# Performance work log

Hardware: AMD Instinct MI355X
Metric: run time of the kernel (lower is better)

## Reference

```python
import jax, jax.numpy as jnp
import numpy as np

N_NODES = 50000
N_EDGES = 800000
D_FEAT = 64
HIDDEN = 128
OUT = 16


def sage_conv(x, src, dst, W_l, W_r, b):
    # PyG SAGEConv (aggr='mean', root_weight=True):
    #   out = lin_l(mean_{j in N(i)} x_j) + lin_r(x_i)
    n = x.shape[0]
    msg = x[src]                                        # [E, d] gather
    agg = jax.ops.segment_sum(msg, dst, num_segments=n) # [N, d]
    deg = jax.ops.segment_sum(jnp.ones((src.shape[0],), x.dtype), dst, num_segments=n)
    mean = agg / jnp.maximum(deg, 1.0)[:, None]         # 0 for isolated nodes
    return mean @ W_l + b + x @ W_r


def setup_inputs() -> dict:
    key = jax.random.key(0)
    ks = jax.random.split(key, 8)
    s = lambda d: 1.0 / np.sqrt(d)
    return {
        "x": jax.random.normal(ks[0], (N_NODES, D_FEAT), dtype=jnp.float32),
        "edge_index": jax.random.randint(ks[1], (2, N_EDGES), 0, N_NODES, dtype=jnp.int32),
        "W1_l": jax.random.normal(ks[2], (D_FEAT, HIDDEN), dtype=jnp.float32) * s(D_FEAT),
        "W1_r": jax.random.normal(ks[3], (D_FEAT, HIDDEN), dtype=jnp.float32) * s(D_FEAT),
        "b1": jnp.zeros((HIDDEN,), dtype=jnp.float32),
        "W2_l": jax.random.normal(ks[4], (HIDDEN, OUT), dtype=jnp.float32) * s(HIDDEN),
        "W2_r": jax.random.normal(ks[5], (HIDDEN, OUT), dtype=jnp.float32) * s(HIDDEN),
        "b2": jnp.zeros((OUT,), dtype=jnp.float32),
    }


def reference(x, edge_index, W1_l, W1_r, b1, W2_l, W2_r, b2):
    src, dst = edge_index[0], edge_index[1]
    h = jax.nn.relu(sage_conv(x, src, dst, W1_l, W1_r, b1))
    h = sage_conv(h, src, dst, W2_l, W2_r, b2)
    # eval-mode path of the original module
    return jax.nn.softmax(h, axis=1)
```

## Files before the change

### kernel.cpp

```cpp
#include <hip/hip_runtime.h>
#include <math.h>

#define N_NODES 50000
#define N_EDGES 800000
#define D_FEAT  64
#define HIDDEN  128
#define OUT     16
#define CAP     64
#define NXCD    8
#define DPG     (N_NODES / NXCD)
#define CSTR    32
#define ABLK    ((N_EDGES / 4 + 255) / 256 * NXCD)
#define PBLK    800

typedef unsigned short ushort_t;
typedef unsigned int uint_t;
typedef __attribute__((ext_vector_type(8))) __bf16 bf16x8;
typedef __attribute__((ext_vector_type(8))) _Float16 half8;
typedef __attribute__((ext_vector_type(4))) float f32x4;

__device__ __forceinline__ void split8(const float* u, bf16x8& ah, bf16x8& al) {
    #pragma unroll
    for (int i = 0; i < 8; ++i) {
        const __bf16 h = (__bf16)u[i];
        ah[i] = h;
        al[i] = (__bf16)(u[i] - (float)h);
    }
}

__global__ __launch_bounds__(256) void prep0_kernel(
        const int* __restrict__ ei,
        uint_t* __restrict__ ep,
        int* __restrict__ cnt) {
    const int idx = blockIdx.x * 256 + threadIdx.x;
    if (idx < N_NODES * CSTR / 4) {
        const int4 z4 = {0, 0, 0, 0};
        ((int4*)cnt)[idx] = z4;
    }
    if (idx < N_EDGES / 4) {
        const int e4 = idx * 4;
        const int4 s = *(const int4*)(ei + e4);
        const int4 d = *(const int4*)(ei + N_EDGES + e4);
        uint4 p;
        p.x = (uint_t)s.x | ((uint_t)d.x << 16);
        p.y = (uint_t)s.y | ((uint_t)d.y << 16);
        p.z = (uint_t)s.z | ((uint_t)d.z << 16);
        p.w = (uint_t)s.w | ((uint_t)d.w << 16);
        *(uint4*)(ep + e4) = p;
    }
}

__global__ __launch_bounds__(256) void mega_kernel(
        const uint_t* __restrict__ ep,
        int* __restrict__ cnt,
        ushort_t* __restrict__ adj,
        const float* __restrict__ x,
        const float* __restrict__ W1l, const float* __restrict__ W1r,
        const float* __restrict__ W2l, const float* __restrict__ W2r,
        _Float16* __restrict__ xh,
        __bf16* __restrict__ Whi1, __bf16* __restrict__ Wlo1,
        __bf16* __restrict__ Whi2, __bf16* __restrict__ Wlo2) {
    const int blk = blockIdx.x;
    if (blk < ABLK) {
        const int g = blk & (NXCD - 1);
        const int b = blk >> 3;
        const int e4 = (b * 256 + threadIdx.x) * 4;
        if (e4 >= N_EDGES) return;
        const uint4 v = *(const uint4*)(ep + e4);
        const uint_t lo = (uint_t)(g * DPG), hi = lo + DPG;
#define PUT(U) { \
        const uint_t d_ = (U) >> 16; \
        if (d_ >= lo && d_ < hi) { \
            int p = atomicAdd(&cnt[d_ * CSTR], 1); \
            if (p < CAP) adj[d_ * CAP + p] = (ushort_t)((U) & 0xFFFFu); \
        } }
        PUT(v.x) PUT(v.y) PUT(v.z) PUT(v.w)
#undef PUT
        return;
    }
    const int idx = (blk - ABLK) * 256 + threadIdx.x;
    if (idx < N_NODES * D_FEAT / 16) {
        const float4* xp = (const float4*)(x + idx * 16);
        const float4 a = xp[0], b = xp[1], c = xp[2], d = xp[3];
        half8 h0, h1;
        h0[0] = (_Float16)a.x; h0[1] = (_Float16)a.y; h0[2] = (_Float16)a.z; h0[3] = (_Float16)a.w;
        h0[4] = (_Float16)b.x; h0[5] = (_Float16)b.y; h0[6] = (_Float16)b.z; h0[7] = (_Float16)b.w;
        h1[0] = (_Float16)c.x; h1[1] = (_Float16)c.y; h1[2] = (_Float16)c.z; h1[3] = (_Float16)c.w;
        h1[4] = (_Float16)d.x; h1[5] = (_Float16)d.y; h1[6] = (_Float16)d.z; h1[7] = (_Float16)d.w;
        *(half8*)(xh + idx * 16) = h0;
        *(half8*)(xh + idx * 16 + 8) = h1;
    }
    if (idx < 16384) {
        const int k = idx >> 7, c = idx & 127;
        const float v = (k < 64) ? W1l[k * HIDDEN + c] : W1r[(k - 64) * HIDDEN + c];
        const int kt = k >> 5, g = (k >> 3) & 3, j = k & 7;
        const int pos = (((kt * 8 + (c >> 4)) * 64) + (g * 16 + (c & 15))) * 8 + j;
        const __bf16 h = (__bf16)v;
        Whi1[pos] = h;
        Wlo1[pos] = (__bf16)(v - (float)h);
    } else if (idx < 20480) {
        const int i2 = idx - 16384;
        const int k = i2 >> 5, c = i2 & 31;
        const float v = (c < 16) ? W2l[k * OUT + c] : W2r[k * OUT + (c - 16)];
        const int kt = k >> 5, g = (k >> 3) & 3, j = k & 7;
        const int pos = (((kt * 2 + (c >> 4)) * 64) + (g * 16 + (c & 15))) * 8 + j;
        const __bf16 h = (__bf16)v;
        Whi2[pos] = h;
        Wlo2[pos] = (__bf16)(v - (float)h);
    }
}

__global__ __launch_bounds__(256) void gather_mean_kernel(
        const _Float16* __restrict__ xh,
        const ushort_t* __restrict__ adj,
        const int* __restrict__ cnt,
        _Float16* __restrict__ meanh) {
    const int w = (blockIdx.x * 256 + threadIdx.x) >> 6;
    if (w >= N_NODES) return;
    const int lane = threadIdx.x & 63;
    const int eg = lane >> 3, fq = lane & 7;
    int deg = cnt[w * CSTR];
    if (deg > CAP) deg = CAP;
    const int start = w * CAP;
    float acc[8];
    #pragma unroll
    for (int i = 0; i < 8; ++i) acc[i] = 0.f;
    int j = eg;
    for (; j + 8 < deg; j += 16) {
        const int s0 = adj[start + j], s1 = adj[start + j + 8];
        const half8 v0 = *(const half8*)(xh + s0 * D_FEAT + 8 * fq);
        const half8 v1 = *(const half8*)(xh + s1 * D_FEAT + 8 * fq);
        #pragma unroll
        for (int i = 0; i < 8; ++i) acc[i] += (float)v0[i] + (float)v1[i];
    }
    if (j < deg) {
        const int s0 = adj[start + j];
        const half8 v0 = *(const half8*)(xh + s0 * D_FEAT + 8 * fq);
        #pragma unroll
        for (int i = 0; i < 8; ++i) acc[i] += (float)v0[i];
    }
    #pragma unroll
    for (int off = 32; off >= 8; off >>= 1) {
        #pragma unroll
        for (int i = 0; i < 8; ++i) acc[i] += __shfl_down(acc[i], off);
    }
    if (lane < 8) {
        const float invd = 1.f / fmaxf((float)deg, 1.f);
        half8 o;
        #pragma unroll
        for (int i = 0; i < 8; ++i) o[i] = (_Float16)(acc[i] * invd);
        *(half8*)(meanh + w * D_FEAT + 8 * fq) = o;
    }
}

__global__ __launch_bounds__(256) void mfma1_kernel(
        const float* __restrict__ x,
        const _Float16* __restrict__ meanh,
        const __bf16* __restrict__ Whi1, const __bf16* __restrict__ Wlo1,
        const __bf16* __restrict__ Whi2, const __bf16* __restrict__ Wlo2,
        const float* __restrict__ b1,
        float* __restrict__ z, float* __restrict__ rbuf) {
    __shared__ float Hs[4][16][132];
    const int w = threadIdx.x >> 6;
    const int l = threadIdx.x & 63;
    const int g = l >> 4;
    const int col = l & 15;
    const int nodebase = blockIdx.x * 64 + w * 16;
    const int nA = nodebase + col;

    f32x4 acc[8];
    #pragma unroll
    for (int ct = 0; ct < 8; ++ct) acc[ct] = (f32x4){0.f, 0.f, 0.f, 0.f};

    #pragma unroll
    for (int kt = 0; kt < 4; ++kt) {
        float u[8];
        #pragma unroll
        for (int i = 0; i < 8; ++i) u[i] = 0.f;
        if (nA < N_NODES) {
            if (kt < 2) {
                const half8 hv = *(const half8*)(meanh + (size_t)nA * 64 + kt * 32 + g * 8);
                #pragma unroll
                for (int i = 0; i < 8; ++i) u[i] = (float)hv[i];
            } else {
                const float* p = x + (size_t)nA * 64 + (kt & 1) * 32 + g * 8;
                const float4 u0 = *(const float4*)p;
                const float4 u1 = *(const float4*)(p + 4);
                u[0] = u0.x; u[1] = u0.y; u[2] = u0.z; u[3] = u0.w;
                u[4] = u1.x; u[5] = u1.y; u[6] = u1.z; u[7] = u1.w;
            }
        }
        bf16x8 ah, al;
        split8(u, ah, al);
        #pragma unroll
        for (int ct = 0; ct < 8; ++ct) {
            const int fo = ((kt * 8 + ct) * 64 + l) * 8;
            const bf16x8 bh = *(const bf16x8*)(Whi1 + fo);
            const bf16x8 bl = *(const bf16x8*)(Wlo1 + fo);
            acc[ct] = __builtin_amdgcn_mfma_f32_16x16x32_bf16(ah, bh, acc[ct], 0, 0, 0);
            acc[ct] = __builtin_amdgcn_mfma_f32_16x16x32_bf16(al, bh, acc[ct], 0, 0, 0);
            acc[ct] = __builtin_amdgcn_mfma_f32_16x16x32_bf16(ah, bl, acc[ct], 0, 0, 0);
        }
    }

    #pragma unroll
    for (int ct = 0; ct < 8; ++ct) {
        const float bv = b1[ct * 16 + col];
        #pragma unroll
        for (int i = 0; i < 4; ++i)
            Hs[w][g * 4 + i][ct * 16 + col] = fmaxf(acc[ct][i] + bv, 0.f);
    }

    f32x4 acc2[2];
    acc2[0] = (f32x4){0.f, 0.f, 0.f, 0.f};
    acc2[1] = (f32x4){0.f, 0.f, 0.f, 0.f};
    #pragma unroll
    for (int kt2 = 0; kt2 < 4; ++kt2) {
        const float* hp = &Hs[w][col][kt2 * 32 + g * 8];
        const float4 u0 = *(const float4*)hp;
        const float4 u1 = *(const float4*)(hp + 4);
        float u[8];
        u[0] = u0.x; u[1] = u0.y; u[2] = u0.z; u[3] = u0.w;
        u[4] = u1.x; u[5] = u1.y; u[6] = u1.z; u[7] = u1.w;
        bf16x8 ah, al;
        split8(u, ah, al);
        #pragma unroll
        for (int ct2 = 0; ct2 < 2; ++ct2) {
            const int fo = ((kt2 * 2 + ct2) * 64 + l) * 8;
            const bf16x8 bh = *(const bf16x8*)(Whi2 + fo);
            const bf16x8 bl = *(const bf16x8*)(Wlo2 + fo);
            acc2[ct2] = __builtin_amdgcn_mfma_f32_16x16x32_bf16(ah, bh, acc2[ct2], 0, 0, 0);
            acc2[ct2] = __builtin_amdgcn_mfma_f32_16x16x32_bf16(al, bh, acc2[ct2], 0, 0, 0);
            acc2[ct2] = __builtin_amdgcn_mfma_f32_16x16x32_bf16(ah, bl, acc2[ct2], 0, 0, 0);
        }
    }
    #pragma unroll
    for (int ct2 = 0; ct2 < 2; ++ct2) {
        float* dst = ct2 ? rbuf : z;
        #pragma unroll
        for (int i = 0; i < 4; ++i) {
            const int node = nodebase + g * 4 + i;
            if (node < N_NODES) dst[node * OUT + col] = acc2[ct2][i];
        }
    }
}

__global__ __launch_bounds__(256) void fused2_kernel(
        const float* __restrict__ z,
        const float* __restrict__ r_in,
        const ushort_t* __restrict__ adj,
        const int* __restrict__ cnt,
        const float* __restrict__ b2,
        float* __restrict__ out) {
    const int w = (blockIdx.x * 256 + threadIdx.x) >> 6;
    if (w >= N_NODES) return;
    const int lane = threadIdx.x & 63;
    const int eg = lane >> 2, kq = lane & 3;
    int deg = cnt[w * CSTR];
    if (deg > CAP) deg = CAP;
    const int start = w * CAP;
    float4 acc = {0.f, 0.f, 0.f, 0.f};
    for (int j = eg; j < deg; j += 16) {
        const float4 v = *(const float4*)(z + adj[start + j] * OUT + 4 * kq);
        acc.x += v.x; acc.y += v.y; acc.z += v.z; acc.w += v.w;
    }
    #pragma unroll
    for (int off = 32; off >= 4; off >>= 1) {
        acc.x += __shfl_down(acc.x, off); acc.y += __shfl_down(acc.y, off);
        acc.z += __shfl_down(acc.z, off); acc.w += __shfl_down(acc.w, off);
    }
    const float invd = 1.f / fmaxf((float)deg, 1.f);
    const float4 rv = *(const float4*)(r_in + w * OUT + 4 * (lane & 3));
    const float4 bv = *(const float4*)(b2 + 4 * (lane & 3));
    float4 s;
    s.x = acc.x * invd + rv.x + bv.x;
    s.y = acc.y * invd + rv.y + bv.y;
    s.z = acc.z * invd + rv.z + bv.z;
    s.w = acc.w * invd + rv.w + bv.w;
    float m = fmaxf(fmaxf(s.x, s.y), fmaxf(s.z, s.w));
    m = fmaxf(m, __shfl_xor(m, 1));
    m = fmaxf(m, __shfl_xor(m, 2));
    float4 e;
    e.x = __expf(s.x - m); e.y = __expf(s.y - m);
    e.z = __expf(s.z - m); e.w = __expf(s.w - m);
    float t = e.x + e.y + e.z + e.w;
    t += __shfl_xor(t, 1);
    t += __shfl_xor(t, 2);
    if (lane < 4) {
        const float it = 1.f / t;
        float4 o;
        o.x = e.x * it; o.y = e.y * it; o.z = e.z * it; o.w = e.w * it;
        *(float4*)(out + w * OUT + 4 * lane) = o;
    }
}

extern "C" void kernel_launch(void* const* d_in, const int* in_sizes, int n_in,
                              void* d_out, int out_size, void* d_ws, size_t ws_size,
                              hipStream_t stream) {
    const float* x   = (const float*)d_in[0];
    const int*   ei  = (const int*)d_in[1];
    const float* W1l = (const float*)d_in[2];
    const float* W1r = (const float*)d_in[3];
    const float* b1  = (const float*)d_in[4];
    const float* W2l = (const float*)d_in[5];
    const float* W2r = (const float*)d_in[6];
    const float* b2  = (const float*)d_in[7];
    float* out = (float*)d_out;

    char* wsB = (char*)d_ws;
    int*       cnt   = (int*)wsB;
    ushort_t*  adj   = (ushort_t*)(wsB + 6400000);
    uint_t*    ep    = (uint_t*)(wsB + 12800000);
    float*     z     = (float*)(wsB + 12800000);
    _Float16*  xh    = (_Float16*)(wsB + 16000000);
    float*     rbuf  = (float*)(wsB + 16000000);
    _Float16*  meanh = (_Float16*)(wsB + 22400000);
    __bf16*    Whi1  = (__bf16*)(wsB + 28800000);
    __bf16*    Wlo1  = Whi1 + 16384;
    __bf16*    Whi2  = Wlo1 + 16384;
    __bf16*    Wlo2  = Whi2 + 4096;

    prep0_kernel<<<(N_NODES * CSTR / 4 + 255) / 256, 256, 0, stream>>>(ei, ep, cnt);
    mega_kernel<<<ABLK + PBLK, 256, 0, stream>>>(ep, cnt, adj, x,
                                                 W1l, W1r, W2l, W2r,
                                                 xh, Whi1, Wlo1, Whi2, Wlo2);
    gather_mean_kernel<<<N_NODES / 4, 256, 0, stream>>>(xh, adj, cnt, meanh);
    mfma1_kernel<<<(N_NODES + 63) / 64, 256, 0, stream>>>(
        x, meanh, Whi1, Wlo1, Whi2, Wlo2, b1, z, rbuf);
    fused2_kernel<<<N_NODES / 4, 256, 0, stream>>>(z, rbuf, adj, cnt, b2, out);
}
```

Before: 105.9 us.

## Build adjacency with LDS atomics over node groups and per-segment slots

Adjacency construction changes from global atomics on strided per-node counters to blocks that each own a group of 782 destination nodes and one eighth of the edges. Degrees are counted with shared-memory atomics and written as per-segment byte counts, so the counter zeroing in prep0 goes away. Each node gets 8 segments of 16 slots, and the gather kernels walk these segment lists. The risk is that every block now scans a whole edge segment (64 groups re-read the edge array), and edges beyond 16 per segment are dropped, which may be rarer or more common than overflow of the old 64-slot cap.

```diff
diff --git a/kernel.cpp b/kernel.cpp
--- a/kernel.cpp
+++ b/kernel.cpp
@@ -6,14 +6,18 @@
 #define D_FEAT  64
 #define HIDDEN  128
 #define OUT     16
-#define CAP     64
-#define NXCD    8
-#define DPG     (N_NODES / NXCD)
-#define CSTR    32
-#define ABLK    ((N_EDGES / 4 + 255) / 256 * NXCD)
+
+#define GROUPS  64
+#define GNODES  782
+#define SPLITE  8
+#define CAPE    16
+#define ESEG    (N_EDGES / SPLITE)
+#define SBLK    (GROUPS * SPLITE)
 #define PBLK    800
+#define ASTR    (SPLITE * CAPE)
 
 typedef unsigned short ushort_t;
+typedef unsigned char uchar_t;
 typedef unsigned int uint_t;
 typedef __attribute__((ext_vector_type(8))) __bf16 bf16x8;
 typedef __attribute__((ext_vector_type(8))) _Float16 half8;
@@ -30,13 +34,8 @@
 
 __global__ __launch_bounds__(256) void prep0_kernel(
         const int* __restrict__ ei,
-        uint_t* __restrict__ ep,
-        int* __restrict__ cnt) {
+        uint_t* __restrict__ ep) {
     const int idx = blockIdx.x * 256 + threadIdx.x;
-    if (idx < N_NODES * CSTR / 4) {
-        const int4 z4 = {0, 0, 0, 0};
-        ((int4*)cnt)[idx] = z4;
-    }
     if (idx < N_EDGES / 4) {
         const int e4 = idx * 4;
         const int4 s = *(const int4*)(ei + e4);
@@ -52,7 +51,7 @@
 
 __global__ __launch_bounds__(256) void mega_kernel(
         const uint_t* __restrict__ ep,
-        int* __restrict__ cnt,
+        uchar_t* __restrict__ cnt8,
         ushort_t* __restrict__ adj,
         const float* __restrict__ x,
         const float* __restrict__ W1l, const float* __restrict__ W1r,
@@ -61,24 +60,37 @@
         __bf16* __restrict__ Whi1, __bf16* __restrict__ Wlo1,
         __bf16* __restrict__ Whi2, __bf16* __restrict__ Wlo2) {
     const int blk = blockIdx.x;
-    if (blk < ABLK) {
-        const int g = blk & (NXCD - 1);
-        const int b = blk >> 3;
-        const int e4 = (b * 256 + threadIdx.x) * 4;
-        if (e4 >= N_EDGES) return;
-        const uint4 v = *(const uint4*)(ep + e4);
-        const uint_t lo = (uint_t)(g * DPG), hi = lo + DPG;
+    if (blk < SBLK) {
+        __shared__ int scnt[GNODES];
+        const int g = blk >> 3;
+        const int e = blk & 7;
+        const int lo = g * GNODES;
+        const int span = ((N_NODES - lo) < GNODES) ? (N_NODES - lo) : GNODES;
+        for (int i = threadIdx.x; i < GNODES; i += 256) scnt[i] = 0;
+        __syncthreads();
+        const uint4* ep4 = (const uint4*)(ep + e * ESEG);
+        for (int i = threadIdx.x; i < ESEG / 4; i += 256) {
+            const uint4 v = ep4[i];
 #define PUT(U) { \
-        const uint_t d_ = (U) >> 16; \
-        if (d_ >= lo && d_ < hi) { \
-            int p = atomicAdd(&cnt[d_ * CSTR], 1); \
-            if (p < CAP) adj[d_ * CAP + p] = (ushort_t)((U) & 0xFFFFu); \
-        } }
-        PUT(v.x) PUT(v.y) PUT(v.z) PUT(v.w)
+            const int d_ = (int)((U) >> 16) - lo; \
+            if ((uint_t)d_ < (uint_t)span) { \
+                const int s_ = atomicAdd(&scnt[d_], 1); \
+                if (s_ < CAPE) \
+                    adj[(size_t)(lo + d_) * ASTR + e * CAPE + s_] = \
+                        (ushort_t)((U) & 0xFFFFu); \
+            } }
+            PUT(v.x) PUT(v.y) PUT(v.z) PUT(v.w)
 #undef PUT
+        }
+        __syncthreads();
+        for (int i = threadIdx.x; i < span; i += 256) {
+            int c = scnt[i];
+            if (c > CAPE) c = CAPE;
+            cnt8[(size_t)(lo + i) * SPLITE + e] = (uchar_t)c;
+        }
         return;
     }
-    const int idx = (blk - ABLK) * 256 + threadIdx.x;
+    const int idx = (blk - SBLK) * 256 + threadIdx.x;
     if (idx < N_NODES * D_FEAT / 16) {
         const float4* xp = (const float4*)(x + idx * 16);
         const float4 a = xp[0], b = xp[1], c = xp[2], d = xp[3];
@@ -93,8 +105,8 @@
     if (idx < 16384) {
         const int k = idx >> 7, c = idx & 127;
         const float v = (k < 64) ? W1l[k * HIDDEN + c] : W1r[(k - 64) * HIDDEN + c];
-        const int kt = k >> 5, g = (k >> 3) & 3, j = k & 7;
-        const int pos = (((kt * 8 + (c >> 4)) * 64) + (g * 16 + (c & 15))) * 8 + j;
+        const int kt = k >> 5, gg = (k >> 3) & 3, j = k & 7;
+        const int pos = (((kt * 8 + (c >> 4)) * 64) + (gg * 16 + (c & 15))) * 8 + j;
         const __bf16 h = (__bf16)v;
         Whi1[pos] = h;
         Wlo1[pos] = (__bf16)(v - (float)h);
@@ -102,8 +114,8 @@
         const int i2 = idx - 16384;
         const int k = i2 >> 5, c = i2 & 31;
         const float v = (c < 16) ? W2l[k * OUT + c] : W2r[k * OUT + (c - 16)];
-        const int kt = k >> 5, g = (k >> 3) & 3, j = k & 7;
-        const int pos = (((kt * 2 + (c >> 4)) * 64) + (g * 16 + (c & 15))) * 8 + j;
+        const int kt = k >> 5, gg = (k >> 3) & 3, j = k & 7;
+        const int pos = (((kt * 2 + (c >> 4)) * 64) + (gg * 16 + (c & 15))) * 8 + j;
         const __bf16 h = (__bf16)v;
         Whi2[pos] = h;
         Wlo2[pos] = (__bf16)(v - (float)h);
@@ -113,31 +125,26 @@
 __global__ __launch_bounds__(256) void gather_mean_kernel(
         const _Float16* __restrict__ xh,
         const ushort_t* __restrict__ adj,
-        const int* __restrict__ cnt,
+        const uchar_t* __restrict__ cnt8,
         _Float16* __restrict__ meanh) {
     const int w = (blockIdx.x * 256 + threadIdx.x) >> 6;
     if (w >= N_NODES) return;
     const int lane = threadIdx.x & 63;
     const int eg = lane >> 3, fq = lane & 7;
-    int deg = cnt[w * CSTR];
-    if (deg > CAP) deg = CAP;
-    const int start = w * CAP;
+    const uint2 cu = *(const uint2*)(cnt8 + (size_t)w * SPLITE);
+    const uint_t cw = (eg < 4) ? cu.x : cu.y;
+    const int ce = (cw >> ((eg & 3) * 8)) & 0xFF;
+    const int deg = (cu.x & 0xFF) + ((cu.x >> 8) & 0xFF) + ((cu.x >> 16) & 0xFF) + (cu.x >> 24)
+                  + (cu.y & 0xFF) + ((cu.y >> 8) & 0xFF) + ((cu.y >> 16) & 0xFF) + (cu.y >> 24);
+    const ushort_t* ab = adj + (size_t)w * ASTR + eg * CAPE;
     float acc[8];
     #pragma unroll
     for (int i = 0; i < 8; ++i) acc[i] = 0.f;
-    int j = eg;
-    for (; j + 8 < deg; j += 16) {
-        const int s0 = adj[start + j], s1 = adj[start + j + 8];
-        const half8 v0 = *(const half8*)(xh + s0 * D_FEAT + 8 * fq);
-        const half8 v1 = *(const half8*)(xh + s1 * D_FEAT + 8 * fq);
-        #pragma unroll
-        for (int i = 0; i < 8; ++i) acc[i] += (float)v0[i] + (float)v1[i];
-    }
-    if (j < deg) {
-        const int s0 = adj[start + j];
-        const half8 v0 = *(const half8*)(xh + s0 * D_FEAT + 8 * fq);
-        #pragma unroll
-        for (int i = 0; i < 8; ++i) acc[i] += (float)v0[i];
+    for (int j = 0; j < ce; ++j) {
+        const int s = ab[j];
+        const half8 v = *(const half8*)(xh + s * D_FEAT + 8 * fq);
+        #pragma unroll
+        for (int i = 0; i < 8; ++i) acc[i] += (float)v[i];
     }
     #pragma unroll
     for (int off = 32; off >= 8; off >>= 1) {
@@ -249,19 +256,23 @@
         const float* __restrict__ z,
         const float* __restrict__ r_in,
         const ushort_t* __restrict__ adj,
-        const int* __restrict__ cnt,
+        const uchar_t* __restrict__ cnt8,
         const float* __restrict__ b2,
         float* __restrict__ out) {
     const int w = (blockIdx.x * 256 + threadIdx.x) >> 6;
     if (w >= N_NODES) return;
     const int lane = threadIdx.x & 63;
     const int eg = lane >> 2, kq = lane & 3;
-    int deg = cnt[w * CSTR];
-    if (deg > CAP) deg = CAP;
-    const int start = w * CAP;
+    const int seg = eg >> 1, j0 = eg & 1;
+    const uint2 cu = *(const uint2*)(cnt8 + (size_t)w * SPLITE);
+    const uint_t cw = (seg < 4) ? cu.x : cu.y;
+    const int ce = (cw >> ((seg & 3) * 8)) & 0xFF;
+    const int deg = (cu.x & 0xFF) + ((cu.x >> 8) & 0xFF) + ((cu.x >> 16) & 0xFF) + (cu.x >> 24)
+                  + (cu.y & 0xFF) + ((cu.y >> 8) & 0xFF) + ((cu.y >> 16) & 0xFF) + (cu.y >> 24);
+    const ushort_t* ab = adj + (size_t)w * ASTR + seg * CAPE;
     float4 acc = {0.f, 0.f, 0.f, 0.f};
-    for (int j = eg; j < deg; j += 16) {
-        const float4 v = *(const float4*)(z + adj[start + j] * OUT + 4 * kq);
+    for (int j = j0; j < ce; j += 2) {
+        const float4 v = *(const float4*)(z + ab[j] * OUT + 4 * kq);
         acc.x += v.x; acc.y += v.y; acc.z += v.z; acc.w += v.w;
     }
     #pragma unroll
@@ -308,24 +319,24 @@
     float* out = (float*)d_out;
 
     char* wsB = (char*)d_ws;
-    int*       cnt   = (int*)wsB;
-    ushort_t*  adj   = (ushort_t*)(wsB + 6400000);
-    uint_t*    ep    = (uint_t*)(wsB + 12800000);
-    float*     z     = (float*)(wsB + 12800000);
-    _Float16*  xh    = (_Float16*)(wsB + 16000000);
-    float*     rbuf  = (float*)(wsB + 16000000);
-    _Float16*  meanh = (_Float16*)(wsB + 22400000);
-    __bf16*    Whi1  = (__bf16*)(wsB + 28800000);
+    uchar_t*   cnt8  = (uchar_t*)wsB;
+    ushort_t*  adj   = (ushort_t*)(wsB + 400000);
+    uint_t*    ep    = (uint_t*)(wsB + 13200000);
+    float*     z     = (float*)(wsB + 13200000);
+    _Float16*  xh    = (_Float16*)(wsB + 16400000);
+    float*     rbuf  = (float*)(wsB + 16400000);
+    _Float16*  meanh = (_Float16*)(wsB + 22800000);
+    __bf16*    Whi1  = (__bf16*)(wsB + 29200000);
     __bf16*    Wlo1  = Whi1 + 16384;
     __bf16*    Whi2  = Wlo1 + 16384;
     __bf16*    Wlo2  = Whi2 + 4096;
 
-    prep0_kernel<<<(N_NODES * CSTR / 4 + 255) / 256, 256, 0, stream>>>(ei, ep, cnt);
-    mega_kernel<<<ABLK + PBLK, 256, 0, stream>>>(ep, cnt, adj, x,
+    prep0_kernel<<<(N_EDGES / 4 + 255) / 256, 256, 0, stream>>>(ei, ep);
+    mega_kernel<<<SBLK + PBLK, 256, 0, stream>>>(ep, cnt8, adj, x,
                                                  W1l, W1r, W2l, W2r,
                                                  xh, Whi1, Wlo1, Whi2, Wlo2);
-    gather_mean_kernel<<<N_NODES / 4, 256, 0, stream>>>(xh, adj, cnt, meanh);
+    gather_mean_kernel<<<N_NODES / 4, 256, 0, stream>>>(xh, adj, cnt8, meanh);
     mfma1_kernel<<<(N_NODES + 63) / 64, 256, 0, stream>>>(
         x, meanh, Whi1, Wlo1, Whi2, Wlo2, b1, z, rbuf);
-    fused2_kernel<<<N_NODES / 4, 256, 0, stream>>>(z, rbuf, adj, cnt, b2, out);
-}
+    fused2_kernel<<<N_NODES / 4, 256, 0, stream>>>(z, rbuf, adj, cnt8, b2, out);
+}
```

After: 128.2 us. +21.0%, slower.

## Replace global-atomic adjacency build with two-pass LDS bucketed binning

Applied to the files above, without the earlier changes.

Builds the CSR-like adjacency in two passes: edge chunks are first binned by destination bucket of 512 nodes using shared-memory counters, then one block per bucket scatters edges into per-node slots with LDS atomics. This removes the padded global count array, its zeroing pass, and the 8x replicated edge scan with global atomics. The trade-off is fixed per-chunk bucket capacity (CCAP=72), which can drop edges if a chunk's bucket overflows, and only 98 blocks doing the second pass, which limits parallelism.

```diff
diff --git a/kernel.cpp b/kernel.cpp
--- a/kernel.cpp
+++ b/kernel.cpp
@@ -7,10 +7,12 @@
 #define HIDDEN  128
 #define OUT     16
 #define CAP     64
-#define NXCD    8
-#define DPG     (N_NODES / NXCD)
-#define CSTR    32
-#define ABLK    ((N_EDGES / 4 + 255) / 256 * NXCD)
+
+#define NBUCK   98
+#define BUCKB   512
+#define NBINA   256
+#define EPB     (N_EDGES / NBINA)
+#define CCAP    72
 #define PBLK    800
 
 typedef unsigned short ushort_t;
@@ -28,32 +30,10 @@
     }
 }
 
-__global__ __launch_bounds__(256) void prep0_kernel(
+__global__ __launch_bounds__(256) void binA_kernel(
         const int* __restrict__ ei,
-        uint_t* __restrict__ ep,
-        int* __restrict__ cnt) {
-    const int idx = blockIdx.x * 256 + threadIdx.x;
-    if (idx < N_NODES * CSTR / 4) {
-        const int4 z4 = {0, 0, 0, 0};
-        ((int4*)cnt)[idx] = z4;
-    }
-    if (idx < N_EDGES / 4) {
-        const int e4 = idx * 4;
-        const int4 s = *(const int4*)(ei + e4);
-        const int4 d = *(const int4*)(ei + N_EDGES + e4);
-        uint4 p;
-        p.x = (uint_t)s.x | ((uint_t)d.x << 16);
-        p.y = (uint_t)s.y | ((uint_t)d.y << 16);
-        p.z = (uint_t)s.z | ((uint_t)d.z << 16);
-        p.w = (uint_t)s.w | ((uint_t)d.w << 16);
-        *(uint4*)(ep + e4) = p;
-    }
-}
-
-__global__ __launch_bounds__(256) void mega_kernel(
-        const uint_t* __restrict__ ep,
-        int* __restrict__ cnt,
-        ushort_t* __restrict__ adj,
+        int* __restrict__ bcntG,
+        uint_t* __restrict__ ebuf,
         const float* __restrict__ x,
         const float* __restrict__ W1l, const float* __restrict__ W1r,
         const float* __restrict__ W2l, const float* __restrict__ W2r,
@@ -61,24 +41,29 @@
         __bf16* __restrict__ Whi1, __bf16* __restrict__ Wlo1,
         __bf16* __restrict__ Whi2, __bf16* __restrict__ Wlo2) {
     const int blk = blockIdx.x;
-    if (blk < ABLK) {
-        const int g = blk & (NXCD - 1);
-        const int b = blk >> 3;
-        const int e4 = (b * 256 + threadIdx.x) * 4;
-        if (e4 >= N_EDGES) return;
-        const uint4 v = *(const uint4*)(ep + e4);
-        const uint_t lo = (uint_t)(g * DPG), hi = lo + DPG;
-#define PUT(U) { \
-        const uint_t d_ = (U) >> 16; \
-        if (d_ >= lo && d_ < hi) { \
-            int p = atomicAdd(&cnt[d_ * CSTR], 1); \
-            if (p < CAP) adj[d_ * CAP + p] = (ushort_t)((U) & 0xFFFFu); \
-        } }
-        PUT(v.x) PUT(v.y) PUT(v.z) PUT(v.w)
-#undef PUT
+    if (blk < NBINA) {
+        __shared__ int lcur[NBUCK];
+        for (int i = threadIdx.x; i < NBUCK; i += 256) lcur[i] = 0;
+        __syncthreads();
+        const int base = blk * EPB;
+        for (int i = threadIdx.x; i < EPB; i += 256) {
+            const int e = base + i;
+            const uint_t s = (uint_t)ei[e];
+            const uint_t d = (uint_t)ei[N_EDGES + e];
+            const int b = (int)(d >> 9);
+            const int r = atomicAdd(&lcur[b], 1);
+            if (r < CCAP)
+                ebuf[((size_t)b * NBINA + blk) * CCAP + r] = s | (d << 16);
+        }
+        __syncthreads();
+        for (int i = threadIdx.x; i < NBUCK; i += 256) {
+            int c = lcur[i];
+            if (c > CCAP) c = CCAP;
+            bcntG[i * NBINA + blk] = c;
+        }
         return;
     }
-    const int idx = (blk - ABLK) * 256 + threadIdx.x;
+    const int idx = (blk - NBINA) * 256 + threadIdx.x;
     if (idx < N_NODES * D_FEAT / 16) {
         const float4* xp = (const float4*)(x + idx * 16);
         const float4 a = xp[0], b = xp[1], c = xp[2], d = xp[3];
@@ -93,8 +78,8 @@
     if (idx < 16384) {
         const int k = idx >> 7, c = idx & 127;
         const float v = (k < 64) ? W1l[k * HIDDEN + c] : W1r[(k - 64) * HIDDEN + c];
-        const int kt = k >> 5, g = (k >> 3) & 3, j = k & 7;
-        const int pos = (((kt * 8 + (c >> 4)) * 64) + (g * 16 + (c & 15))) * 8 + j;
+        const int kt = k >> 5, gg = (k >> 3) & 3, j = k & 7;
+        const int pos = (((kt * 8 + (c >> 4)) * 64) + (gg * 16 + (c & 15))) * 8 + j;
         const __bf16 h = (__bf16)v;
         Whi1[pos] = h;
         Wlo1[pos] = (__bf16)(v - (float)h);
@@ -102,11 +87,44 @@
         const int i2 = idx - 16384;
         const int k = i2 >> 5, c = i2 & 31;
         const float v = (c < 16) ? W2l[k * OUT + c] : W2r[k * OUT + (c - 16)];
-        const int kt = k >> 5, g = (k >> 3) & 3, j = k & 7;
-        const int pos = (((kt * 2 + (c >> 4)) * 64) + (g * 16 + (c & 15))) * 8 + j;
+        const int kt = k >> 5, gg = (k >> 3) & 3, j = k & 7;
+        const int pos = (((kt * 2 + (c >> 4)) * 64) + (gg * 16 + (c & 15))) * 8 + j;
         const __bf16 h = (__bf16)v;
         Whi2[pos] = h;
         Wlo2[pos] = (__bf16)(v - (float)h);
+    }
+}
+
+__global__ __launch_bounds__(256) void binB_kernel(
+        const uint_t* __restrict__ ebuf,
+        const int* __restrict__ bcntG,
+        ushort_t* __restrict__ adj,
+        int* __restrict__ cnt) {
+    __shared__ int scnt[BUCKB];
+    const int b = blockIdx.x;
+    const int lo = b << 9;
+    for (int i = threadIdx.x; i < BUCKB; i += 256) scnt[i] = 0;
+    __syncthreads();
+    const int wave = threadIdx.x >> 6, lane = threadIdx.x & 63;
+    for (int c = wave; c < NBINA; c += 4) {
+        const int cc = bcntG[b * NBINA + c];
+        const uint_t* eb = ebuf + ((size_t)b * NBINA + c) * CCAP;
+        for (int off = lane; off < cc; off += 64) {
+            const uint_t u = eb[off];
+            const int dl = (int)(u >> 16) - lo;
+            const int s = atomicAdd(&scnt[dl], 1);
+            if (s < CAP)
+                adj[(size_t)(lo + dl) * CAP + s] = (ushort_t)(u & 0xFFFFu);
+        }
+    }
+    __syncthreads();
+    for (int i = threadIdx.x; i < BUCKB; i += 256) {
+        const int node = lo + i;
+        if (node < N_NODES) {
+            int c = scnt[i];
+            if (c > CAP) c = CAP;
+            cnt[node] = c;
+        }
     }
 }
 
@@ -119,8 +137,7 @@
     if (w >= N_NODES) return;
     const int lane = threadIdx.x & 63;
     const int eg = lane >> 3, fq = lane & 7;
-    int deg = cnt[w * CSTR];
-    if (deg > CAP) deg = CAP;
+    const int deg = cnt[w];
     const int start = w * CAP;
     float acc[8];
     #pragma unroll
@@ -256,8 +273,7 @@
     if (w >= N_NODES) return;
     const int lane = threadIdx.x & 63;
     const int eg = lane >> 2, kq = lane & 3;
-    int deg = cnt[w * CSTR];
-    if (deg > CAP) deg = CAP;
+    const int deg = cnt[w];
     const int start = w * CAP;
     float4 acc = {0.f, 0.f, 0.f, 0.f};
     for (int j = eg; j < deg; j += 16) {
@@ -308,22 +324,23 @@
     float* out = (float*)d_out;
 
     char* wsB = (char*)d_ws;
-    int*       cnt   = (int*)wsB;
-    ushort_t*  adj   = (ushort_t*)(wsB + 6400000);
-    uint_t*    ep    = (uint_t*)(wsB + 12800000);
-    float*     z     = (float*)(wsB + 12800000);
-    _Float16*  xh    = (_Float16*)(wsB + 16000000);
-    float*     rbuf  = (float*)(wsB + 16000000);
-    _Float16*  meanh = (_Float16*)(wsB + 22400000);
-    __bf16*    Whi1  = (__bf16*)(wsB + 28800000);
+    int*       bcntG = (int*)wsB;
+    uint_t*    ebuf  = (uint_t*)(wsB + 102400);
+    _Float16*  meanh = (_Float16*)(wsB + 102400);
+    ushort_t*  adj   = (ushort_t*)(wsB + 7327744);
+    int*       cnt   = (int*)(wsB + 13727744);
+    _Float16*  xh    = (_Float16*)(wsB + 13927744);
+    float*     z     = (float*)(wsB + 13927744);
+    float*     rbuf  = (float*)(wsB + 17127744);
+    __bf16*    Whi1  = (__bf16*)(wsB + 20327744);
     __bf16*    Wlo1  = Whi1 + 16384;
     __bf16*    Whi2  = Wlo1 + 16384;
     __bf16*    Wlo2  = Whi2 + 4096;
 
-    prep0_kernel<<<(N_NODES * CSTR / 4 + 255) / 256, 256, 0, stream>>>(ei, ep, cnt);
-    mega_kernel<<<ABLK + PBLK, 256, 0, stream>>>(ep, cnt, adj, x,
-                                                 W1l, W1r, W2l, W2r,
-                                                 xh, Whi1, Wlo1, Whi2, Wlo2);
+    binA_kernel<<<NBINA + PBLK, 256, 0, stream>>>(ei, bcntG, ebuf, x,
+                                                  W1l, W1r, W2l, W2r,
+                                                  xh, Whi1, Wlo1, Whi2, Wlo2);
+    binB_kernel<<<NBUCK, 256, 0, stream>>>(ebuf, bcntG, adj, cnt);
     gather_mean_kernel<<<N_NODES / 4, 256, 0, stream>>>(xh, adj, cnt, meanh);
     mfma1_kernel<<<(N_NODES + 63) / 64, 256, 0, stream>>>(
         x, meanh, Whi1, Wlo1, Whi2, Wlo2, b1, z, rbuf);
```

After: 115.5 us. +9.0%, slower.
